# Kernel optimization log

Measured on AMD Instinct MI355X. Metric: run time of the kernel, lower is better.

## Reference

```python
import jax, jax.numpy as jnp
import numpy as np

N_CLASSES = 18
NMS_PRE = 1000   # test_cfg.nms_pre, per level
K_NMS = 500      # per-class candidates entering greedy NMS
SCORE_THR = 0.01
IOU_THR = 0.5
LEVEL_NS = [600000, 300000, 150000, 75000]


def _decode(points, pred):
    # fcaf3d axis-aligned decode: pred = (dx-, dx+, dy-, dy+, dz-, dz+) >= 0
    cx = points[:, 0] + (pred[:, 1] - pred[:, 0]) / 2
    cy = points[:, 1] + (pred[:, 3] - pred[:, 2]) / 2
    cz = points[:, 2] + (pred[:, 5] - pred[:, 4]) / 2
    w = pred[:, 0] + pred[:, 1]
    l = pred[:, 2] + pred[:, 3]
    h = pred[:, 4] + pred[:, 5]
    return jnp.stack([cx, cy, cz, w, l, h], axis=-1)  # [N, 6]


def _iou3d(b):
    # axis-aligned 3D IoU, b: [K,6] (cx,cy,cz,w,l,h) -> [K,K]
    mn = b[:, :3] - b[:, 3:] / 2
    mx = b[:, :3] + b[:, 3:] / 2
    lt = jnp.maximum(mn[:, None, :], mn[None, :, :])
    rb = jnp.minimum(mx[:, None, :], mx[None, :, :])
    inter = jnp.clip(rb - lt, 0.0).prod(-1)
    vol = jnp.clip(mx - mn, 0.0).prod(-1)
    return inter / (vol[:, None] + vol[None, :] - inter + 1e-6)


def _level(centerness, bbox_pred, cls_score, points):
    # fused score: cls.sigmoid() * centerness.sigmoid()
    scores = jax.nn.sigmoid(cls_score) * jax.nn.sigmoid(centerness)  # [N,C]
    max_scores = scores.max(axis=1)
    _, ids = jax.lax.top_k(max_scores, NMS_PRE)  # per-level prefilter
    bboxes = _decode(points[ids], bbox_pred[ids])  # [NMS_PRE, 6]
    return bboxes, scores[ids]


def _nms_class(boxes, scores):
    # boxes [M,6], scores [M] for one class -> greedy NMS on top K_NMS
    valid = scores > SCORE_THR
    s = jnp.where(valid, scores, -1.0)
    sv, order = jax.lax.top_k(s, K_NMS)  # sorted desc
    b = boxes[order]
    v = sv > SCORE_THR
    iou = _iou3d(b)  # [K,K]
    idx = jnp.arange(K_NMS)

    def body(i, sup):
        alive = jnp.logical_not(sup[i])
        return sup | (alive & (iou[i] > IOU_THR) & (idx > i))

    sup = jax.lax.fori_loop(0, K_NMS, body, jnp.logical_not(v))
    keep = jnp.logical_not(sup) & v
    return b, sv, keep


def _forward(levels):
    mlvl_bboxes, mlvl_scores = [], []
    for (cn, bp, cs, pt) in levels:
        b, s = _level(cn, bp, cs, pt)
        mlvl_bboxes.append(b)
        mlvl_scores.append(s)
    bboxes = jnp.concatenate(mlvl_bboxes)  # [4*NMS_PRE, 6]
    scores = jnp.concatenate(mlvl_scores)  # [4*NMS_PRE, C]
    # per-class NMS (vmap over class dim)
    b, sv, keep = jax.vmap(_nms_class, in_axes=(None, 1))(bboxes, scores)
    labels = jnp.broadcast_to(jnp.arange(N_CLASSES, dtype=jnp.int32)[:, None], sv.shape)
    return (b.reshape(-1, 6), sv.reshape(-1), labels.reshape(-1), keep.reshape(-1))


def setup_inputs() -> dict:
    key = jax.random.key(0)
    out = {}
    for li, n in enumerate(LEVEL_NS):
        k1, k2, k3, k4, key = jax.random.split(key, 5)
        out[f'centerness{li}'] = jax.random.normal(k1, (n, 1), jnp.float32)
        out[f'bbox_pred{li}'] = jax.random.uniform(k2, (n, 6), jnp.float32)  # non-negative distances
        out[f'cls_score{li}'] = jax.random.normal(k3, (n, N_CLASSES), jnp.float32)
        out[f'points{li}'] = jax.random.normal(k4, (n, 3), jnp.float32) * 2.0
    return out


def reference(centerness0, bbox_pred0, cls_score0, points0,
              centerness1, bbox_pred1, cls_score1, points1,
              centerness2, bbox_pred2, cls_score2, points2,
              centerness3, bbox_pred3, cls_score3, points3):
    levels = [
        (centerness0, bbox_pred0, cls_score0, points0),
        (centerness1, bbox_pred1, cls_score1, points1),
        (centerness2, bbox_pred2, cls_score2, points2),
        (centerness3, bbox_pred3, cls_score3, points3),
    ]
    return _forward(levels)
```

## Files before the change

### kernel.cpp

```cpp
#include <hip/hip_runtime.h>
#include <math.h>

#define N_CLASSES 18
#define NMS_PRE   1000
#define K_NMS     500
#define POOL      4000
#define LIST_CAP  2048
#define NREP      16
#define NSUB      16
#define SUBCAP    (LIST_CAP/NSUB)
#define IOU_THR   0.5f
#define SCORE_THR 0.01f

typedef unsigned long long ull;

struct Ptrs {
  const float* cent[4];
  const float* bbox[4];
  const float* cls[4];
  const float* pts[4];
  int off[4];
  int ntot;
};

__device__ __forceinline__ unsigned int fsort(float f){
  unsigned int b = __float_as_uint(f);
  return (b & 0x80000000u) ? ~b : (b | 0x80000000u);
}
__device__ __forceinline__ float fsort_inv(unsigned int k){
  unsigned int b = (k & 0x80000000u) ? (k & 0x7FFFFFFFu) : ~k;
  return __uint_as_float(b);
}
__device__ __forceinline__ float sigmoidf_(float x){
  return 1.0f / (1.0f + expf(-x));
}
__device__ __forceinline__ int level_of(int f, const Ptrs& P){
  return (f >= P.off[3]) ? 3 : (f >= P.off[2]) ? 2 : (f >= P.off[1]) ? 1 : 0;
}

__device__ __forceinline__ ull cx_keep(ull mine, ull part, bool keep_hi){
  ull mx = mine > part ? mine : part;
  ull mn = mine > part ? part : mine;
  return keep_hi ? mx : mn;
}
__device__ __forceinline__ void cxpair(ull &a, ull &b, bool a_hi){
  ull mx = a > b ? a : b;
  ull mn = a > b ? b : a;
  a = a_hi ? mx : mn;
  b = a_hi ? mn : mx;
}

__global__ void __launch_bounds__(256) init_kernel(unsigned int* hist_rep){
  int tid = blockIdx.x*256 + threadIdx.x;
  int stride = gridDim.x*256;
  for (int j = tid; j < NREP*4*2048; j += stride) hist_rep[j] = 0u;
}

__global__ void __launch_bounds__(512) compute_keys(Ptrs P, unsigned int* keys,
                        unsigned int* hist_rep){
  __shared__ unsigned int lh[2048];
  int t = threadIdx.x;
  for (int j = t; j < 2048; j += 512) lh[j] = 0u;
  int ip = blockIdx.x*512 + t;
  int f  = ip << 1;
  int rep = blockIdx.x & (NREP - 1);
  bool valid = f < P.ntot;
  int f0 = blockIdx.x << 10;
  int fL = min(f0 + 1023, P.ntot - 1);
  bool uni = (level_of(f0, P) == level_of(fL, P)) && (f0 + 1023 < P.ntot);
  int Lb = level_of(f0, P);

  float mA = 0.f, mB = 0.f, cA = 0.f, cB = 0.f;
  int L = 0;
  if (valid){
    L = level_of(f, P);
    int i = f - P.off[L];
    const float4* q = (const float4*)(P.cls[L] + (size_t)i * N_CLASSES);
    float4 q0 = q[0], q1 = q[1], q2 = q[2], q3 = q[3], q4 = q[4];
    float4 q5 = q[5], q6 = q[6], q7 = q[7], q8 = q[8];
    mA = fmaxf(fmaxf(fmaxf(q0.x,q0.y), fmaxf(q0.z,q0.w)),
         fmaxf(fmaxf(fmaxf(q1.x,q1.y), fmaxf(q1.z,q1.w)),
         fmaxf(fmaxf(fmaxf(q2.x,q2.y), fmaxf(q2.z,q2.w)),
         fmaxf(fmaxf(fmaxf(q3.x,q3.y), fmaxf(q3.z,q3.w)),
               fmaxf(q4.x,q4.y)))));
    mB = fmaxf(fmaxf(q4.z,q4.w),
         fmaxf(fmaxf(fmaxf(q5.x,q5.y), fmaxf(q5.z,q5.w)),
         fmaxf(fmaxf(fmaxf(q6.x,q6.y), fmaxf(q6.z,q6.w)),
         fmaxf(fmaxf(fmaxf(q7.x,q7.y), fmaxf(q7.z,q7.w)),
               fmaxf(fmaxf(q8.x,q8.y), fmaxf(q8.z,q8.w))))));
    const float2 c2 = *(const float2*)(P.cent[L] + i);
    cA = c2.x; cB = c2.y;
  }
  __syncthreads();

  if (valid){
    float sA = sigmoidf_(mA) * sigmoidf_(cA);
    float sB = sigmoidf_(mB) * sigmoidf_(cB);
    unsigned int kA = fsort(sA), kB = fsort(sB);
    *(uint2*)(keys + f) = make_uint2(kA, kB);
    if (uni){
      atomicAdd(&lh[kA >> 21], 1u);
      atomicAdd(&lh[kB >> 21], 1u);
    } else {
      unsigned int* hb = hist_rep + ((rep*4) + L)*2048;
      atomicAdd(&hb[kA >> 21], 1u);
      atomicAdd(&hb[kB >> 21], 1u);
    }
  }
  __syncthreads();
  if (uni){
    unsigned int* hb = hist_rep + ((rep*4) + Lb)*2048;
    for (int j = t; j < 2048; j += 512){
      unsigned int v = lh[j];
      if (v) atomicAdd(&hb[j], v);
    }
  }
}

__global__ void __launch_bounds__(512) hist_level(Ptrs P, const unsigned int* keys,
                        const unsigned int* state, unsigned int* hist2){
  int ip = blockIdx.x*512 + threadIdx.x;
  int f = ip << 1;
  if (f < P.ntot){
    int L = level_of(f, P);
    uint2 kk = *(const uint2*)(keys + f);
    unsigned int Pfx = state[2*L];
    unsigned int hi = Pfx >> 21;
    if ((kk.x >> 21) == hi) atomicAdd(&hist2[L*2048 + ((kk.x >> 10) & 0x7FFu)], 1u);
    if ((kk.y >> 21) == hi) atomicAdd(&hist2[L*2048 + ((kk.y >> 10) & 0x7FFu)], 1u);
  }
}

__global__ void __launch_bounds__(256) scan_sel(const unsigned int* src, int nrep,
                        unsigned int* state, int pass,
                        unsigned int* hist2z, ull* listsz, unsigned int* scntz){
  __shared__ unsigned int lhist[2048];
  int L = blockIdx.x, t = threadIdx.x;
  if (pass == 0){
    for (int j = t; j < 2048; j += 256) hist2z[L*2048 + j] = 0u;
  } else {
    for (int j = t; j < LIST_CAP; j += 256) listsz[(size_t)L*LIST_CAP + j] = 0ull;
    if (t < NSUB) scntz[(L*NSUB + t)*16] = 0u;
  }
  for (int j = t; j < 2048; j += 256){
    unsigned int s = 0u;
    if (nrep == NREP){
#pragma unroll
      for (int r = 0; r < NREP; ++r) s += src[((r*4) + L)*2048 + j];
    } else {
      s = src[L*2048 + j];
    }
    lhist[j] = s;
  }
  __syncthreads();
  if (t < 64){
    int lane = t;
    unsigned int krem = (pass == 0) ? NMS_PRE : state[2*L + 1];
    unsigned int Pfx  = (pass == 0) ? 0u      : state[2*L];
    unsigned int carry = 0;
    for (int ch = 0; ch < 32; ++ch){
      unsigned int cnt = lhist[2047 - (ch*64 + lane)];
      unsigned int pfx = cnt;
#pragma unroll
      for (int off = 1; off < 64; off <<= 1){
        unsigned int u = __shfl_up(pfx, off);
        if (lane >= off) pfx += u;
      }
      unsigned int C = carry + pfx;
      ull bal = __ballot(C >= krem);
      if (bal){
        int fl2 = __ffsll(bal) - 1;
        unsigned int Cf = __shfl(C, fl2);
        unsigned int cf = __shfl(cnt, fl2);
        if (lane == 0){
          unsigned int b = (unsigned int)(2047 - (ch*64 + fl2));
          state[2*L]     = (pass == 0) ? (b << 21) : (Pfx | (b << 10));
          state[2*L + 1] = krem - (Cf - cf);
        }
        break;
      }
      carry = __shfl(C, 63);
    }
  }
}

__global__ void __launch_bounds__(512) compact_kernel(Ptrs P, const unsigned int* keys,
                        const unsigned int* state, unsigned int* scnt, ull* lists){
  int ip = blockIdx.x*512 + threadIdx.x;
  int f = ip << 1;
  if (f >= P.ntot) return;
  int L = level_of(f, P);
  uint2 kk = *(const uint2*)(keys + f);
  unsigned int T = state[2*L];
  unsigned int sub = (unsigned int)blockIdx.x & (NSUB - 1);
  if (kk.x >= T){
    unsigned int pos = atomicAdd(&scnt[(L*NSUB + sub)*16], 1u);
    if (pos < SUBCAP){
      unsigned int i = (unsigned int)(f - P.off[L]);
      lists[(size_t)L*LIST_CAP + sub*SUBCAP + pos] = ((ull)kk.x << 32) | (ull)(~i);
    }
  }
  if (kk.y >= T){
    unsigned int pos = atomicAdd(&scnt[(L*NSUB + sub)*16], 1u);
    if (pos < SUBCAP){
      unsigned int i = (unsigned int)(f + 1 - P.off[L]);
      lists[(size_t)L*LIST_CAP + sub*SUBCAP + pos] = ((ull)kk.y << 32) | (ull)(~i);
    }
  }
}

__global__ void __launch_bounds__(1024) sort_gather(Ptrs P, const ull* lists,
                        float* boxes_pool, float* scores_pool){
  __shared__ ull buf[LIST_CAP];
  int L = blockIdx.x;
  int t = threadIdx.x;
  int e1 = t + 1024;
  const ull* src = lists + (size_t)L*LIST_CAP;
  ull v0 = src[t];
  ull v1 = src[e1];
  for (int k = 2; k <= 2048; k <<= 1){
    for (int j = k >> 1; j > 0; j >>= 1){
      bool hi0 = (((t  & j) == 0) == ((t  & k) == 0));
      bool hi1 = (((e1 & j) == 0) == ((e1 & k) == 0));
      if (j >= 1024){
        cxpair(v0, v1, hi0);
      } else if (j >= 64){
        __syncthreads();
        buf[t] = v0; buf[e1] = v1;
        __syncthreads();
        ull p0 = buf[t ^ j];
        ull p1 = buf[e1 ^ j];
        v0 = cx_keep(v0, p0, hi0);
        v1 = cx_keep(v1, p1, hi1);
      } else {
        ull p0 = __shfl_xor(v0, j);
        ull p1 = __shfl_xor(v1, j);
        v0 = cx_keep(v0, p0, hi0);
        v1 = cx_keep(v1, p1, hi1);
      }
    }
  }
  if (t < NMS_PRE){
    unsigned int i = ~((unsigned int)(v0 & 0xFFFFFFFFu));
    int r = L*NMS_PRE + t;
    const float* bp = P.bbox[L] + (size_t)i * 6;
    const float* pp = P.pts[L]  + (size_t)i * 3;
    float p0 = bp[0], p1 = bp[1], p2 = bp[2], p3 = bp[3], p4 = bp[4], p5 = bp[5];
    float cx = pp[0] + (p1 - p0) * 0.5f;
    float cy = pp[1] + (p3 - p2) * 0.5f;
    float cz = pp[2] + (p5 - p4) * 0.5f;
    float w = p0 + p1, l = p2 + p3, h = p4 + p5;
    float* bo = boxes_pool + (size_t)r * 6;
    bo[0] = cx; bo[1] = cy; bo[2] = cz; bo[3] = w; bo[4] = l; bo[5] = h;
    float cs = sigmoidf_(P.cent[L][i]);
    const float* cl = P.cls[L] + (size_t)i * N_CLASSES;
#pragma unroll
    for (int c = 0; c < N_CLASSES; ++c)
      scores_pool[(size_t)c * POOL + r] = sigmoidf_(cl[c]) * cs;
  }
}

__global__ void __launch_bounds__(1024) class_topk(const float* scores_pool, const float* boxes_pool,
                        float* out, float* aabb){
  __shared__ unsigned int keyS[4096];
  __shared__ ull comp[512];
  __shared__ unsigned int histS[256];
  __shared__ unsigned int wsum[16], wpre[16];
  __shared__ unsigned int sP, sK, sCnt;
  int c = blockIdx.x;
  int t = threadIdx.x;
  int w = t >> 6, lane = t & 63;

  for (int j = t; j < 4096; j += 1024){
    unsigned int k = 0u;
    if (j < POOL){
      float s = scores_pool[(size_t)c*POOL + j];
      float sval = (s > SCORE_THR) ? s : -1.0f;
      k = fsort(sval);
    }
    keyS[j] = k;
  }
  if (t == 0){ sP = 0u; sK = K_NMS; sCnt = 0u; }
  __syncthreads();

  for (int pass = 0; pass < 4; ++pass){
    int shift = 24 - 8*pass;
    if (t < 256) histS[t] = 0u;
    __syncthreads();
    unsigned int Pfx = sP;
    for (int j = t; j < 4096; j += 1024){
      unsigned int k = keyS[j];
      if ((((ull)(k ^ Pfx)) >> (shift + 8)) == 0ull)
        atomicAdd(&histS[(k >> shift) & 0xFFu], 1u);
    }
    __syncthreads();
    if (w == 0){
      unsigned int krem = sK;
      unsigned int carry = 0;
      for (int ch = 0; ch < 4; ++ch){
        unsigned int cnt = histS[255 - (ch*64 + lane)];
        unsigned int pfx = cnt;
#pragma unroll
        for (int off = 1; off < 64; off <<= 1){
          unsigned int u = __shfl_up(pfx, off);
          if (lane >= off) pfx += u;
        }
        unsigned int C = carry + pfx;
        ull bal = __ballot(C >= krem);
        if (bal){
          int fl = __ffsll(bal) - 1;
          unsigned int Cf = __shfl(C, fl);
          unsigned int cf = __shfl(cnt, fl);
          if (lane == 0){
            sP = Pfx | ((unsigned int)(255 - (ch*64 + fl)) << shift);
            sK = krem - (Cf - cf);
          }
          break;
        }
        carry = __shfl(C, 63);
      }
    }
    __syncthreads();
  }
  unsigned int T = sP, need = sK;

  unsigned int loc[4]; unsigned int ct = 0;
#pragma unroll
  for (int q = 0; q < 4; ++q){
    unsigned int k = keyS[4*t + q];
    loc[q] = k;
    ct += (k == T) ? 1u : 0u;
  }
  unsigned int inc = ct;
#pragma unroll
  for (int off = 1; off < 64; off <<= 1){
    unsigned int u = __shfl_up(inc, off);
    if (lane >= off) inc += u;
  }
  if (lane == 63) wsum[w] = inc;
  __syncthreads();
  if (t < 16){
    unsigned int v = wsum[t];
    unsigned int pincl = v;
#pragma unroll
    for (int off = 1; off < 16; off <<= 1){
      unsigned int u = __shfl_up(pincl, off);
      if (t >= off) pincl += u;
    }
    wpre[t] = pincl - v;
  }
  __syncthreads();
  unsigned int excl = wpre[w] + (inc - ct);

#pragma unroll
  for (int q = 0; q < 4; ++q){
    unsigned int k = loc[q];
    bool surv = false;
    if (k > T) surv = true;
    else if (k == T){ surv = (excl < need); excl += 1u; }
    if (surv){
      unsigned int pos = atomicAdd(&sCnt, 1u);
      if (pos < 512)
        comp[pos] = ((ull)k << 32) | (ull)(~(unsigned int)(4*t + q));
    }
  }
  __syncthreads();

  ull v0 = 0ull;
  if (t < 512 && t < (int)sCnt) v0 = comp[t];
  for (int k = 2; k <= 512; k <<= 1){
    for (int j = k >> 1; j > 0; j >>= 1){
      if (j >= 64){
        __syncthreads();
        if (t < 512) comp[t] = v0;
        __syncthreads();
        if (t < 512){
          ull p0 = comp[t ^ j];
          bool hi0 = (((t & j) == 0) == ((t & k) == 0));
          v0 = cx_keep(v0, p0, hi0);
        }
      } else {
        if (t < 512){
          ull p0 = __shfl_xor(v0, j);
          bool hi0 = (((t & j) == 0) == ((t & k) == 0));
          v0 = cx_keep(v0, p0, hi0);
        }
      }
    }
  }

  if (t < K_NMS){
    ull cm = v0;
    unsigned int j = ~((unsigned int)(cm & 0xFFFFFFFFu));
    float sval = fsort_inv((unsigned int)(cm >> 32));
    int o = c*K_NMS + t;
    const float* bp = boxes_pool + (size_t)j * 6;
    float b0 = bp[0], b1 = bp[1], b2 = bp[2], b3 = bp[3], b4 = bp[4], b5 = bp[5];
    float* ob = out + (size_t)o * 6;
    ob[0] = b0; ob[1] = b1; ob[2] = b2; ob[3] = b3; ob[4] = b4; ob[5] = b5;
    out[54000 + o] = sval;
    out[63000 + o] = (float)c;
    float mn0 = b0 - b3*0.5f, mx0 = b0 + b3*0.5f;
    float mn1 = b1 - b4*0.5f, mx1 = b1 + b4*0.5f;
    float mn2 = b2 - b5*0.5f, mx2 = b2 + b5*0.5f;
    float vol = fmaxf(mx0 - mn0, 0.f) * fmaxf(mx1 - mn1, 0.f) * fmaxf(mx2 - mn2, 0.f);
    float* ap = aabb + ((size_t)c*512 + t) * 8;
    ap[0] = mn0; ap[1] = mn1; ap[2] = mn2; ap[3] = mx0; ap[4] = mx1; ap[5] = mx2;
    ap[6] = vol; ap[7] = sval;
  }
}

__global__ void __launch_bounds__(512) nms_mask(const float* aabb, ull* maskG, ull* flagsG){
  __shared__ float smn0[512], smn1[512], smn2[512];
  __shared__ float smx0[512], smx1[512], smx2[512];
  __shared__ float svol[512];
  __shared__ ull rowbuf[64*8];
  int c = blockIdx.y, chunk = blockIdx.x;
  int t = threadIdx.x, w = t >> 6, lane = t & 63;
  float mn0 = 0.f, mn1 = 0.f, mn2 = 0.f, mx0 = 0.f, mx1 = 0.f, mx2 = 0.f, vol = 0.f;
  if (t < K_NMS){
    const float* ap = aabb + ((size_t)c*512 + t) * 8;
    mn0 = ap[0]; mn1 = ap[1]; mn2 = ap[2];
    mx0 = ap[3]; mx1 = ap[4]; mx2 = ap[5]; vol = ap[6];
  }
  smn0[t] = mn0; smn1[t] = mn1; smn2[t] = mn2;
  smx0[t] = mx0; smx1[t] = mx1; smx2[t] = mx2;
  svol[t] = vol;
  __syncthreads();
  int i0 = chunk * 64, i1 = min(i0 + 64, K_NMS);
  for (int i = i0; i < i1; ++i){
    float lt0 = fmaxf(smn0[i], mn0), lt1 = fmaxf(smn1[i], mn1), lt2 = fmaxf(smn2[i], mn2);
    float rb0 = fminf(smx0[i], mx0), rb1 = fminf(smx1[i], mx1), rb2 = fminf(smx2[i], mx2);
    float inter = fmaxf(rb0 - lt0, 0.f) * fmaxf(rb1 - lt1, 0.f) * fmaxf(rb2 - lt2, 0.f);
    float denom = svol[i] + vol - inter + 1e-6f;
    bool s = (t < K_NMS) && (t > i) && (inter / denom > IOU_THR);
    ull m = __ballot(s);
    if (lane == 0){
      maskG[((size_t)c*K_NMS + i)*8 + w] = m;
      rowbuf[(i - i0)*8 + w] = m;
    }
  }
  __syncthreads();
  if (t < 64){
    int r = i0 + t;
    bool nz = false;
    if (r < K_NMS){
      ull o = 0ull;
#pragma unroll
      for (int z = 0; z < 8; ++z) o |= rowbuf[t*8 + z];
      nz = (o != 0ull);
    }
    ull bal = __ballot(nz);
    if (t == 0) flagsG[(size_t)c*8 + chunk] = bal;
  }
}

__global__ void __launch_bounds__(512) nms_greedy(const float* aabb, const ull* maskG,
                        const ull* flagsG, float* keep_out){
  __shared__ ull maskS[K_NMS*8];
  __shared__ ull vbitsS[8], remS[8];
  int c = blockIdx.x, t = threadIdx.x, w = t >> 6, lane = t & 63;
  ull flg[8];
#pragma unroll
  for (int q = 0; q < 8; ++q) flg[q] = flagsG[(size_t)c*8 + q];
  for (int j = t; j < K_NMS*8; j += 512) maskS[j] = maskG[(size_t)c*K_NMS*8 + j];
  float sv = (t < K_NMS) ? aabb[((size_t)c*512 + t)*8 + 7] : -1.0f;
  ull vb = __ballot(sv > SCORE_THR);
  if (lane == 0) vbitsS[w] = vb;
  __syncthreads();
  if (w == 0){
    ull rem[8];
#pragma unroll
    for (int q = 0; q < 8; ++q) rem[q] = ~vbitsS[q];
#pragma unroll
    for (int q = 0; q < 8; ++q){
      ull cand = flg[q] & ~rem[q];
      while (cand){
        int b = __ffsll(cand) - 1;
        int i = q*64 + b;
#pragma unroll
        for (int z = 0; z < 8; ++z) rem[z] |= maskS[i*8 + z];
        ull above = (b < 63) ? (~0ull << (b + 1)) : 0ull;
        cand = flg[q] & ~rem[q] & above;
      }
    }
    if (lane == 0){
#pragma unroll
      for (int q = 0; q < 8; ++q) remS[q] = rem[q];
    }
  }
  __syncthreads();
  if (t < K_NMS)
    keep_out[c*K_NMS + t] = ((remS[t >> 6] >> (t & 63)) & 1ull) ? 0.0f : 1.0f;
}

extern "C" void kernel_launch(void* const* d_in, const int* in_sizes, int n_in,
                              void* d_out, int out_size, void* d_ws, size_t ws_size,
                              hipStream_t stream){
  Ptrs P;
  int off = 0;
  for (int L = 0; L < 4; ++L){
    P.cent[L] = (const float*)d_in[4*L + 0];
    P.bbox[L] = (const float*)d_in[4*L + 1];
    P.cls[L]  = (const float*)d_in[4*L + 2];
    P.pts[L]  = (const float*)d_in[4*L + 3];
    P.off[L]  = off;
    off += in_sizes[4*L + 0];
  }
  P.ntot = off;

  char* w = (char*)d_ws;
  size_t o = 0;
  auto alloc = [&](size_t bytes) -> char* {
    char* p = w + o;
    o = (o + bytes + 255) & ~(size_t)255;
    return p;
  };
  unsigned int* keys        = (unsigned int*)alloc((size_t)P.ntot * 4);
  unsigned int* hist_rep    = (unsigned int*)alloc((size_t)NREP * 4 * 2048 * 4);
  unsigned int* hist2       = (unsigned int*)alloc(4 * 2048 * 4);
  unsigned int* state       = (unsigned int*)alloc(4 * 2 * 4);
  unsigned int* scnt        = (unsigned int*)alloc(4 * NSUB * 16 * 4);
  ull* lists                = (ull*)alloc((size_t)4 * LIST_CAP * 8);
  float* boxes_pool         = (float*)alloc((size_t)POOL * 6 * 4);
  float* scores_pool        = (float*)alloc((size_t)N_CLASSES * POOL * 4);
  float* aabb               = (float*)alloc((size_t)N_CLASSES * 512 * 8 * 4);
  ull* maskG                = (ull*)alloc((size_t)N_CLASSES * K_NMS * 8 * 8);
  ull* flagsG               = (ull*)alloc((size_t)N_CLASSES * 8 * 8);

  float* out = (float*)d_out;
  int npairs = P.ntot >> 1;
  int pgrid = (npairs + 511) / 512;

  init_kernel<<<64, 256, 0, stream>>>(hist_rep);
  compute_keys<<<pgrid, 512, 0, stream>>>(P, keys, hist_rep);
  scan_sel<<<4, 256, 0, stream>>>(hist_rep, NREP, state, 0, hist2, lists, scnt);
  hist_level<<<pgrid, 512, 0, stream>>>(P, keys, state, hist2);
  scan_sel<<<4, 256, 0, stream>>>(hist2, 1, state, 1, hist2, lists, scnt);
  compact_kernel<<<pgrid, 512, 0, stream>>>(P, keys, state, scnt, lists);
  sort_gather<<<4, 1024, 0, stream>>>(P, lists, boxes_pool, scores_pool);
  class_topk<<<N_CLASSES, 1024, 0, stream>>>(scores_pool, boxes_pool, out, aabb);
  nms_mask<<<dim3(8, N_CLASSES), 512, 0, stream>>>(aabb, maskG, flagsG);
  nms_greedy<<<N_CLASSES, 512, 0, stream>>>(aabb, maskG, flagsG, out + 72000);
}
```

Measured before the change: 281.9 us.

## Fuse class top-k with NMS mask and greedy; split gather into wide kernel

Merges class_topk, nms_mask and nms_greedy into one kernel per class. The IoU suppression mask now stays in shared memory instead of round-tripping through global buffers, which also removes two launches. The gather and decode step moves out of the 4-block sort kernel into a separate 63-block kernel so the scattered loads are spread over more CUs. In exchange, the mask for each class is built by a single 1024-thread block rather than 8 blocks, and the fused kernel uses more shared memory.

New measurement: 305.5 us. 8.4% more time.

```diff
diff --git a/kernel.cpp b/kernel.cpp
--- a/kernel.cpp
+++ b/kernel.cpp
@@ -209,8 +209,7 @@
   }
 }
 
-__global__ void __launch_bounds__(1024) sort_gather(Ptrs P, const ull* lists,
-                        float* boxes_pool, float* scores_pool){
+__global__ void __launch_bounds__(1024) sort_idx(const ull* lists, unsigned int* sidx){
   __shared__ ull buf[LIST_CAP];
   int L = blockIdx.x;
   int t = threadIdx.x;
@@ -240,33 +239,41 @@
       }
     }
   }
-  if (t < NMS_PRE){
-    unsigned int i = ~((unsigned int)(v0 & 0xFFFFFFFFu));
-    int r = L*NMS_PRE + t;
-    const float* bp = P.bbox[L] + (size_t)i * 6;
-    const float* pp = P.pts[L]  + (size_t)i * 3;
-    float p0 = bp[0], p1 = bp[1], p2 = bp[2], p3 = bp[3], p4 = bp[4], p5 = bp[5];
-    float cx = pp[0] + (p1 - p0) * 0.5f;
-    float cy = pp[1] + (p3 - p2) * 0.5f;
-    float cz = pp[2] + (p5 - p4) * 0.5f;
-    float w = p0 + p1, l = p2 + p3, h = p4 + p5;
-    float* bo = boxes_pool + (size_t)r * 6;
-    bo[0] = cx; bo[1] = cy; bo[2] = cz; bo[3] = w; bo[4] = l; bo[5] = h;
-    float cs = sigmoidf_(P.cent[L][i]);
-    const float* cl = P.cls[L] + (size_t)i * N_CLASSES;
-#pragma unroll
-    for (int c = 0; c < N_CLASSES; ++c)
-      scores_pool[(size_t)c * POOL + r] = sigmoidf_(cl[c]) * cs;
-  }
-}
-
-__global__ void __launch_bounds__(1024) class_topk(const float* scores_pool, const float* boxes_pool,
-                        float* out, float* aabb){
-  __shared__ unsigned int keyS[4096];
+  if (t < NMS_PRE) sidx[L*NMS_PRE + t] = ~((unsigned int)(v0 & 0xFFFFFFFFu));
+}
+
+__global__ void __launch_bounds__(64) gather_decode(Ptrs P, const unsigned int* sidx,
+                        float* boxes_pool, float* scores_pool){
+  int r = blockIdx.x*64 + threadIdx.x;
+  if (r >= POOL) return;
+  int L = r / NMS_PRE;
+  unsigned int i = sidx[r];
+  const float* bp = P.bbox[L] + (size_t)i * 6;
+  const float* pp = P.pts[L]  + (size_t)i * 3;
+  float p0 = bp[0], p1 = bp[1], p2 = bp[2], p3 = bp[3], p4 = bp[4], p5 = bp[5];
+  float cx = pp[0] + (p1 - p0) * 0.5f;
+  float cy = pp[1] + (p3 - p2) * 0.5f;
+  float cz = pp[2] + (p5 - p4) * 0.5f;
+  float w = p0 + p1, l = p2 + p3, h = p4 + p5;
+  float* bo = boxes_pool + (size_t)r * 6;
+  bo[0] = cx; bo[1] = cy; bo[2] = cz; bo[3] = w; bo[4] = l; bo[5] = h;
+  float cs = sigmoidf_(P.cent[L][i]);
+  const float* cl = P.cls[L] + (size_t)i * N_CLASSES;
+#pragma unroll
+  for (int c = 0; c < N_CLASSES; ++c)
+    scores_pool[(size_t)c * POOL + r] = sigmoidf_(cl[c]) * cs;
+}
+
+__global__ void __launch_bounds__(1024) class_topk_nms(const float* scores_pool,
+                        const float* boxes_pool, float* out){
+  __shared__ ull maskS[512*8];
   __shared__ ull comp[512];
+  __shared__ float boxA[8][512];
   __shared__ unsigned int histS[256];
   __shared__ unsigned int wsum[16], wpre[16];
+  __shared__ ull vbitsS[8], flgS[8], remS[8];
   __shared__ unsigned int sP, sK, sCnt;
+  unsigned int* keyS = (unsigned int*)&boxA[0][0];
   int c = blockIdx.x;
   int t = threadIdx.x;
   int w = t >> 6, lane = t & 63;
@@ -388,100 +395,85 @@
       }
     }
   }
-
-  if (t < K_NMS){
-    ull cm = v0;
-    unsigned int j = ~((unsigned int)(cm & 0xFFFFFFFFu));
-    float sval = fsort_inv((unsigned int)(cm >> 32));
-    int o = c*K_NMS + t;
-    const float* bp = boxes_pool + (size_t)j * 6;
-    float b0 = bp[0], b1 = bp[1], b2 = bp[2], b3 = bp[3], b4 = bp[4], b5 = bp[5];
-    float* ob = out + (size_t)o * 6;
-    ob[0] = b0; ob[1] = b1; ob[2] = b2; ob[3] = b3; ob[4] = b4; ob[5] = b5;
-    out[54000 + o] = sval;
-    out[63000 + o] = (float)c;
-    float mn0 = b0 - b3*0.5f, mx0 = b0 + b3*0.5f;
-    float mn1 = b1 - b4*0.5f, mx1 = b1 + b4*0.5f;
-    float mn2 = b2 - b5*0.5f, mx2 = b2 + b5*0.5f;
-    float vol = fmaxf(mx0 - mn0, 0.f) * fmaxf(mx1 - mn1, 0.f) * fmaxf(mx2 - mn2, 0.f);
-    float* ap = aabb + ((size_t)c*512 + t) * 8;
-    ap[0] = mn0; ap[1] = mn1; ap[2] = mn2; ap[3] = mx0; ap[4] = mx1; ap[5] = mx2;
-    ap[6] = vol; ap[7] = sval;
-  }
-}
-
-__global__ void __launch_bounds__(512) nms_mask(const float* aabb, ull* maskG, ull* flagsG){
-  __shared__ float smn0[512], smn1[512], smn2[512];
-  __shared__ float smx0[512], smx1[512], smx2[512];
-  __shared__ float svol[512];
-  __shared__ ull rowbuf[64*8];
-  int c = blockIdx.y, chunk = blockIdx.x;
-  int t = threadIdx.x, w = t >> 6, lane = t & 63;
-  float mn0 = 0.f, mn1 = 0.f, mn2 = 0.f, mx0 = 0.f, mx1 = 0.f, mx2 = 0.f, vol = 0.f;
-  if (t < K_NMS){
-    const float* ap = aabb + ((size_t)c*512 + t) * 8;
-    mn0 = ap[0]; mn1 = ap[1]; mn2 = ap[2];
-    mx0 = ap[3]; mx1 = ap[4]; mx2 = ap[5]; vol = ap[6];
-  }
-  smn0[t] = mn0; smn1[t] = mn1; smn2[t] = mn2;
-  smx0[t] = mx0; smx1[t] = mx1; smx2[t] = mx2;
-  svol[t] = vol;
-  __syncthreads();
-  int i0 = chunk * 64, i1 = min(i0 + 64, K_NMS);
-  for (int i = i0; i < i1; ++i){
-    float lt0 = fmaxf(smn0[i], mn0), lt1 = fmaxf(smn1[i], mn1), lt2 = fmaxf(smn2[i], mn2);
-    float rb0 = fminf(smx0[i], mx0), rb1 = fminf(smx1[i], mx1), rb2 = fminf(smx2[i], mx2);
-    float inter = fmaxf(rb0 - lt0, 0.f) * fmaxf(rb1 - lt1, 0.f) * fmaxf(rb2 - lt2, 0.f);
-    float denom = svol[i] + vol - inter + 1e-6f;
-    bool s = (t < K_NMS) && (t > i) && (inter / denom > IOU_THR);
-    ull m = __ballot(s);
-    if (lane == 0){
-      maskG[((size_t)c*K_NMS + i)*8 + w] = m;
-      rowbuf[(i - i0)*8 + w] = m;
-    }
-  }
-  __syncthreads();
-  if (t < 64){
-    int r = i0 + t;
+  __syncthreads();
+
+  if (t < 512){
+    float mn0 = 0.f, mn1 = 0.f, mn2 = 0.f, mx0 = 0.f, mx1 = 0.f, mx2 = 0.f;
+    float vol = 0.f, sval = -1.0f;
+    if (t < K_NMS){
+      unsigned int jj = ~((unsigned int)(v0 & 0xFFFFFFFFu));
+      sval = fsort_inv((unsigned int)(v0 >> 32));
+      int o = c*K_NMS + t;
+      const float* bp = boxes_pool + (size_t)jj * 6;
+      float b0 = bp[0], b1 = bp[1], b2 = bp[2], b3 = bp[3], b4 = bp[4], b5 = bp[5];
+      float* ob = out + (size_t)o * 6;
+      ob[0] = b0; ob[1] = b1; ob[2] = b2; ob[3] = b3; ob[4] = b4; ob[5] = b5;
+      out[54000 + o] = sval;
+      out[63000 + o] = (float)c;
+      mn0 = b0 - b3*0.5f; mx0 = b0 + b3*0.5f;
+      mn1 = b1 - b4*0.5f; mx1 = b1 + b4*0.5f;
+      mn2 = b2 - b5*0.5f; mx2 = b2 + b5*0.5f;
+      vol = fmaxf(mx0 - mn0, 0.f) * fmaxf(mx1 - mn1, 0.f) * fmaxf(mx2 - mn2, 0.f);
+    }
+    boxA[0][t] = mn0; boxA[1][t] = mn1; boxA[2][t] = mn2;
+    boxA[3][t] = mx0; boxA[4][t] = mx1; boxA[5][t] = mx2;
+    boxA[6][t] = vol; boxA[7][t] = sval;
+  }
+  __syncthreads();
+
+  {
+    int col = t & 511;
+    float cmn0 = boxA[0][col], cmn1 = boxA[1][col], cmn2 = boxA[2][col];
+    float cmx0 = boxA[3][col], cmx1 = boxA[4][col], cmx2 = boxA[5][col];
+    float cvol = boxA[6][col];
+    bool colv = (col < K_NMS);
+    int half = t >> 9;
+    int w7 = w & 7;
+    for (int i = 0; i < K_NMS; i += 2){
+      int r = i + half;
+      float rmn0 = boxA[0][r], rmn1 = boxA[1][r], rmn2 = boxA[2][r];
+      float rmx0 = boxA[3][r], rmx1 = boxA[4][r], rmx2 = boxA[5][r];
+      float rvol = boxA[6][r];
+      float lt0 = fmaxf(rmn0, cmn0), lt1 = fmaxf(rmn1, cmn1), lt2 = fmaxf(rmn2, cmn2);
+      float rb0 = fminf(rmx0, cmx0), rb1 = fminf(rmx1, cmx1), rb2 = fminf(rmx2, cmx2);
+      float inter = fmaxf(rb0 - lt0, 0.f) * fmaxf(rb1 - lt1, 0.f) * fmaxf(rb2 - lt2, 0.f);
+      float denom = rvol + cvol - inter + 1e-6f;
+      bool s = colv && (col > r) && (inter / denom > IOU_THR);
+      ull m = __ballot(s);
+      if (lane == 0) maskS[r*8 + w7] = m;
+    }
+  }
+  __syncthreads();
+
+  if (t < 512){
     bool nz = false;
-    if (r < K_NMS){
-      ull o = 0ull;
-#pragma unroll
-      for (int z = 0; z < 8; ++z) o |= rowbuf[t*8 + z];
-      nz = (o != 0ull);
+    if (t < K_NMS){
+      ull o8 = 0ull;
+#pragma unroll
+      for (int z = 0; z < 8; ++z) o8 |= maskS[t*8 + z];
+      nz = (o8 != 0ull);
     }
     ull bal = __ballot(nz);
-    if (t == 0) flagsG[(size_t)c*8 + chunk] = bal;
-  }
-}
-
-__global__ void __launch_bounds__(512) nms_greedy(const float* aabb, const ull* maskG,
-                        const ull* flagsG, float* keep_out){
-  __shared__ ull maskS[K_NMS*8];
-  __shared__ ull vbitsS[8], remS[8];
-  int c = blockIdx.x, t = threadIdx.x, w = t >> 6, lane = t & 63;
-  ull flg[8];
-#pragma unroll
-  for (int q = 0; q < 8; ++q) flg[q] = flagsG[(size_t)c*8 + q];
-  for (int j = t; j < K_NMS*8; j += 512) maskS[j] = maskG[(size_t)c*K_NMS*8 + j];
-  float sv = (t < K_NMS) ? aabb[((size_t)c*512 + t)*8 + 7] : -1.0f;
-  ull vb = __ballot(sv > SCORE_THR);
-  if (lane == 0) vbitsS[w] = vb;
-  __syncthreads();
+    if (lane == 0) flgS[w] = bal;
+    ull vbb = __ballot(boxA[7][t] > SCORE_THR);
+    if (lane == 0) vbitsS[w] = vbb;
+  }
+  __syncthreads();
+
   if (w == 0){
     ull rem[8];
 #pragma unroll
     for (int q = 0; q < 8; ++q) rem[q] = ~vbitsS[q];
 #pragma unroll
     for (int q = 0; q < 8; ++q){
-      ull cand = flg[q] & ~rem[q];
+      ull cand = flgS[q] & ~rem[q];
       while (cand){
         int b = __ffsll(cand) - 1;
         int i = q*64 + b;
 #pragma unroll
         for (int z = 0; z < 8; ++z) rem[z] |= maskS[i*8 + z];
         ull above = (b < 63) ? (~0ull << (b + 1)) : 0ull;
-        cand = flg[q] & ~rem[q] & above;
+        cand = flgS[q] & ~rem[q] & above;
       }
     }
     if (lane == 0){
@@ -491,7 +483,7 @@
   }
   __syncthreads();
   if (t < K_NMS)
-    keep_out[c*K_NMS + t] = ((remS[t >> 6] >> (t & 63)) & 1ull) ? 0.0f : 1.0f;
+    out[72000 + c*K_NMS + t] = ((remS[t >> 6] >> (t & 63)) & 1ull) ? 0.0f : 1.0f;
 }
 
 extern "C" void kernel_launch(void* const* d_in, const int* in_sizes, int n_in,
@@ -522,11 +514,9 @@
   unsigned int* state       = (unsigned int*)alloc(4 * 2 * 4);
   unsigned int* scnt        = (unsigned int*)alloc(4 * NSUB * 16 * 4);
   ull* lists                = (ull*)alloc((size_t)4 * LIST_CAP * 8);
+  unsigned int* sidx        = (unsigned int*)alloc((size_t)POOL * 4);
   float* boxes_pool         = (float*)alloc((size_t)POOL * 6 * 4);
   float* scores_pool        = (float*)alloc((size_t)N_CLASSES * POOL * 4);
-  float* aabb               = (float*)alloc((size_t)N_CLASSES * 512 * 8 * 4);
-  ull* maskG                = (ull*)alloc((size_t)N_CLASSES * K_NMS * 8 * 8);
-  ull* flagsG               = (ull*)alloc((size_t)N_CLASSES * 8 * 8);
 
   float* out = (float*)d_out;
   int npairs = P.ntot >> 1;
@@ -538,8 +528,7 @@
   hist_level<<<pgrid, 512, 0, stream>>>(P, keys, state, hist2);
   scan_sel<<<4, 256, 0, stream>>>(hist2, 1, state, 1, hist2, lists, scnt);
   compact_kernel<<<pgrid, 512, 0, stream>>>(P, keys, state, scnt, lists);
-  sort_gather<<<4, 1024, 0, stream>>>(P, lists, boxes_pool, scores_pool);
-  class_topk<<<N_CLASSES, 1024, 0, stream>>>(scores_pool, boxes_pool, out, aabb);
-  nms_mask<<<dim3(8, N_CLASSES), 512, 0, stream>>>(aabb, maskG, flagsG);
-  nms_greedy<<<N_CLASSES, 512, 0, stream>>>(aabb, maskG, flagsG, out + 72000);
-}
+  sort_idx<<<4, 1024, 0, stream>>>(lists, sidx);
+  gather_decode<<<(POOL + 63)/64, 64, 0, stream>>>(P, sidx, boxes_pool, scores_pool);
+  class_topk_nms<<<N_CLASSES, 1024, 0, stream>>>(scores_pool, boxes_pool, out);
+}
```
